# Kernel tuning notes

Measured on AMD Instinct MI355X. Metric: run time of the kernel, lower is better.

## Reference

```python
import jax, jax.numpy as jnp
import numpy as np

B, C, H, W = 1, 512, 64, 64
HEADS, DIM_HEAD = 8, 64
GROUPS = 32
EPS = 1e-5
SCALE = DIM_HEAD ** -0.5


def setup_inputs() -> dict:
    key = jax.random.key(0)
    ks = jax.random.split(key, 8)
    inner = HEADS * DIM_HEAD  # 512
    s = 0.02
    return {
        "hidden_states": jax.random.normal(ks[0], (B, C, H, W), jnp.float32),
        "gn_gamma": jnp.ones((C,), jnp.float32),
        "gn_beta": jnp.zeros((C,), jnp.float32),
        "wq": jax.random.normal(ks[1], (inner, C), jnp.float32) * s,
        "wk": jax.random.normal(ks[2], (inner, C), jnp.float32) * s,
        "wv": jax.random.normal(ks[3], (inner, C), jnp.float32) * s,
        "wo": jax.random.normal(ks[4], (C, inner), jnp.float32) * s,
        "bo": jnp.zeros((C,), jnp.float32),
    }


def _group_norm(x, gamma, beta):
    # x: [B, C, H, W]; normalize within channel groups over (C//G, H, W)
    b, c, h, w = x.shape
    xg = x.reshape(b, GROUPS, c // GROUPS, h, w)
    mean = xg.mean(axis=(2, 3, 4), keepdims=True)
    var = xg.var(axis=(2, 3, 4), keepdims=True)
    xg = (xg - mean) * jax.lax.rsqrt(var + EPS)
    x = xg.reshape(b, c, h, w)
    return x * gamma[None, :, None, None] + beta[None, :, None, None]


def reference(hidden_states, gn_gamma, gn_beta, wq, wk, wv, wo, bo):
    residual = hidden_states
    x = _group_norm(hidden_states, gn_gamma, gn_beta)
    b, c, h, w = x.shape
    n = h * w
    x = x.reshape(b, c, n).transpose(0, 2, 1)  # [B, N, C]

    # torch Linear: y = x @ W^T (bias=False for q/k/v)
    q = (x @ wq.T).reshape(b, n, HEADS, DIM_HEAD).transpose(0, 2, 1, 3)  # [B,H,N,D]
    k = (x @ wk.T).reshape(b, n, HEADS, DIM_HEAD).transpose(0, 2, 1, 3)
    v = (x @ wv.T).reshape(b, n, HEADS, DIM_HEAD).transpose(0, 2, 1, 3)

    scores = jnp.einsum("bhqd,bhkd->bhqk", q, k) * SCALE  # [B,H,N,N]
    probs = jax.nn.softmax(scores, axis=-1)
    out = jnp.einsum("bhqk,bhkd->bhqd", probs, v)  # [B,H,N,D]

    out = out.transpose(0, 2, 1, 3).reshape(b, n, HEADS * DIM_HEAD)  # [B,N,inner]
    out = out @ wo.T + bo  # [B,N,C]
    out = out.transpose(0, 2, 1).reshape(b, c, h, w)
    return out + residual
```

## Files before the change

### kernel.cpp

```cpp
#include <hip/hip_runtime.h>

#define N_TOK 4096
#define C_DIM 512
#define NH    8
#define EPS   1e-5f
#define NSPLIT 4
#define THR   11.0f

typedef __attribute__((ext_vector_type(8))) __bf16 bf16x8;
typedef __attribute__((ext_vector_type(4))) float  f32x4;
using u16 = unsigned short;
using u32 = unsigned int;

#define MFMA16 __builtin_amdgcn_mfma_f32_16x16x32_bf16

__device__ __forceinline__ u16 f2bf(float f){
  u32 x = __builtin_bit_cast(u32, f);
  x += 0x7fffu + ((x>>16)&1u);
  return (u16)(x>>16);
}
__device__ __forceinline__ float bf2f(u16 v){
  return __builtin_bit_cast(float, (u32)v<<16);
}
__device__ __forceinline__ float exp2a(float x){
  float r; asm("v_exp_f32 %0, %1" : "=v"(r) : "v"(x)); return r;
}
__device__ __forceinline__ u32 cvtpk(float lo, float hi){
  u32 r; asm("v_cvt_pk_bf16_f32 %0, %1, %2" : "=v"(r) : "v"(lo), "v"(hi)); return r;
}
__device__ __forceinline__ float max3a(float a, float b, float c){
  float r; asm("v_max3_f32 %0, %1, %2, %3" : "=v"(r) : "v"(a), "v"(b), "v"(c)); return r;
}
__device__ __forceinline__ void dma16(const void* src, void* lds){
  __builtin_amdgcn_global_load_lds(
      (const __attribute__((address_space(1))) u32*)src,
      (__attribute__((address_space(3))) u32*)lds, 16, 0, 0);
}

__global__ __launch_bounds__(256) void k_pre(const float* __restrict__ s0,
      const float* __restrict__ s1, const float* __restrict__ s2,
      const float* __restrict__ s3, u16* __restrict__ d0, u16* __restrict__ d1,
      u16* __restrict__ d2, u16* __restrict__ d3,
      const float* __restrict__ x, float* __restrict__ pstat,
      u16* __restrict__ xbf){
  __shared__ float rs[4], rss[4];
  int b = blockIdx.x;
  if (b < 1024){
    int m = b >> 8;
    int i = (b & 255)*256 + threadIdx.x;
    const float* s = m==0?s0 : m==1?s1 : m==2?s2 : s3;
    u16*         d = m==0?d0 : m==1?d1 : m==2?d2 : d3;
    float4 v = ((const float4*)s)[i];
    ushort4 o; o.x=f2bf(v.x); o.y=f2bf(v.y); o.z=f2bf(v.z); o.w=f2bf(v.w);
    ((ushort4*)d)[i] = o;
    return;
  }
  int gb = b - 1024;
  int g = gb>>3, p = gb&7, t = threadIdx.x;
  const float4* gx4 = (const float4*)(x + (size_t)g*16*N_TOK) + (size_t)p*2048;
  ushort4* xb4 = (ushort4*)xbf + (size_t)g*16384 + (size_t)p*2048;
  float s=0.f, ss=0.f;
  #pragma unroll
  for (int k=0;k<8;k++){
    float4 v = gx4[t + k*256];
    s  += v.x+v.y+v.z+v.w;
    ss += v.x*v.x+v.y*v.y+v.z*v.z+v.w*v.w;
    ushort4 o; o.x=f2bf(v.x); o.y=f2bf(v.y); o.z=f2bf(v.z); o.w=f2bf(v.w);
    xb4[t + k*256] = o;
  }
  for (int m=1;m<64;m<<=1){ s += __shfl_xor(s,m); ss += __shfl_xor(ss,m); }
  int w=t>>6, lane=t&63;
  if (lane==0){ rs[w]=s; rss[w]=ss; }
  __syncthreads();
  if (t==0){
    pstat[(g*8+p)*2  ] = rs[0]+rs[1]+rs[2]+rs[3];
    pstat[(g*8+p)*2+1] = rss[0]+rss[1]+rss[2]+rss[3];
  }
}

__global__ __launch_bounds__(256) void k_gn_apply(const u16* __restrict__ xbf,
      const float* __restrict__ pstat, const float* __restrict__ gamma,
      const float* __restrict__ beta, u16* __restrict__ X){
  int g = blockIdx.x, c0 = g*16;
  int n = blockIdx.y*256 + threadIdx.x;
  float S=0.f, SS=0.f;
  #pragma unroll
  for (int p=0;p<8;p++){ S += pstat[(g*8+p)*2]; SS += pstat[(g*8+p)*2+1]; }
  float mean = S*(1.f/65536.f);
  float rstd = rsqrtf(SS*(1.f/65536.f) - mean*mean + EPS);
  u16 ov[16];
  #pragma unroll
  for (int c=0;c<16;c++){
    float gm = gamma[c0+c]*rstd;
    float be = beta[c0+c] - mean*gm;
    float v  = bf2f(xbf[(size_t)(c0+c)*N_TOK + n])*gm + be;
    ov[c] = f2bf(v);
  }
  uint4* dst = (uint4*)&X[(size_t)n*C_DIM + c0];
  dst[0] = *(uint4*)&ov[0];
  dst[1] = *(uint4*)&ov[8];
}

__device__ __forceinline__ void gemm_core64(const u16* A, const u16* B,
      int m0, int n0, char* LDS, f32x4 (&acc)[4][2]){
  int t = threadIdx.x, w = t>>6, l = t&63, lr = l&15, li = l>>4;
  int wr = w>>1, wc = w&1;
  char* As = LDS;
  char* Bs = LDS + 32768;
  const char* Ac = (const char*)A + (size_t)m0*1024;
  const char* Bc = (const char*)B + (size_t)n0*1024;
  int rswz = (lr&7)<<4;

  int rowA[4], segA[4], rowB[2], segB[2];
  #pragma unroll
  for (int k=0;k<4;k++){ int s=t+k*256; rowA[k]=s>>3; segA[k]=s&7; }
  #pragma unroll
  for (int k=0;k<2;k++){ int s=t+k*256; rowB[k]=s>>3; segB[k]=s&7; }

  #define STAGE(it, bb) { int koff=(it)*128;                                   \
    _Pragma("unroll")                                                          \
    for (int k=0;k<4;k++){                                                     \
      int ys = (segA[k]*16) ^ ((rowA[k]&7)<<4);                                \
      dma16(Ac + (size_t)rowA[k]*1024 + koff + ys,                             \
            As + (bb)*16384 + w*1024 + k*4096);                                \
    }                                                                          \
    _Pragma("unroll")                                                          \
    for (int k=0;k<2;k++){                                                     \
      int ys = (segB[k]*16) ^ ((rowB[k]&7)<<4);                                \
      dma16(Bc + (size_t)rowB[k]*1024 + koff + ys,                             \
            Bs + (bb)*8192 + w*1024 + k*4096);                                 \
    } }

  STAGE(0, 0);
  __syncthreads();

  int buf = 0;
  for (int it=0; it<8; it++){
    if (it < 7){ STAGE(it+1, buf^1); }
    char* Ab = As + buf*16384;
    char* Bb = Bs + buf*8192;
    #pragma unroll
    for (int ks=0; ks<2; ks++){
      bf16x8 af[4], bfr[2];
      #pragma unroll
      for (int i=0;i<4;i++){
        int ra = wr*64 + i*16 + lr;
        af[i]  = *(const bf16x8*)(Ab + ra*128 + ((li*16 + ks*64) ^ rswz));
      }
      #pragma unroll
      for (int j=0;j<2;j++){
        int rb = wc*32 + j*16 + lr;
        bfr[j] = *(const bf16x8*)(Bb + rb*128 + ((li*16 + ks*64) ^ rswz));
      }
      __builtin_amdgcn_s_setprio(1);
      #pragma unroll
      for (int i=0;i<4;i++){
        #pragma unroll
        for (int j=0;j<2;j++){
          acc[i][j] = MFMA16(af[i], bfr[j], acc[i][j], 0,0,0);
        }
      }
      __builtin_amdgcn_s_setprio(0);
    }
    __syncthreads();
    buf ^= 1;
  }
  #undef STAGE
}

__global__ __launch_bounds__(256,3) void k_qkv2(const u16* __restrict__ X,
      const u16* __restrict__ wq, const u16* __restrict__ wk,
      const u16* __restrict__ wv, u16* __restrict__ Qo, u16* __restrict__ Ko,
      u16* __restrict__ Vto){
  __shared__ char LDS[49152];
  int b = blockIdx.x;
  const u16 *A, *B; u16* Cp; int ldc, m0, n0; float sc = 1.f; bool vperm = false;
  if (b < 256){        A=X;  B=wq; Cp=Qo;  ldc=512;  m0=(b>>3)*128; n0=(b&7)*64;
                       sc = 0.125f*1.44269504f; }
  else if (b < 512){ int r=b-256; A=X;  B=wk; Cp=Ko;  ldc=512;  m0=(r>>3)*128; n0=(r&7)*64; }
  else             { int r=b-512; A=wv; B=X;  Cp=Vto; ldc=4096; m0=(r>>6)*128; n0=(r&63)*64;
                     vperm = true; }

  f32x4 acc[4][2] = {};
  gemm_core64(A, B, m0, n0, LDS, acc);

  int t = threadIdx.x, w = t>>6, l = t&63, lr = l&15, li = l>>4;
  int wr = w>>1, wc = w&1;
  #pragma unroll
  for (int i=0;i<4;i++){
    #pragma unroll
    for (int rr=0;rr<4;rr++){
      int mm = m0 + wr*64 + i*16 + li*4 + rr;
      #pragma unroll
      for (int j=0;j<2;j++){
        int nn = n0 + wc*32 + j*16 + lr;
        if (vperm){
          int tl = nn & 63;
          int pos = (tl & 35) | ((tl & 12) << 1) | ((tl & 16) >> 2);
          nn = (nn & ~63) | pos;
        }
        Cp[(size_t)mm*ldc + nn] = f2bf(acc[i][j][rr]*sc);
      }
    }
  }
}

__global__ __launch_bounds__(256,3) void k_oproj2(const u16* __restrict__ Wo,
      const u16* __restrict__ Ob, const float* __restrict__ bo,
      const float* __restrict__ res, float* __restrict__ out){
  __shared__ char LDS[49152];
  int b = blockIdx.x;
  int m0 = (b>>6)*128, n0 = (b&63)*64;

  f32x4 acc[4][2] = {};
  gemm_core64(Wo, Ob, m0, n0, LDS, acc);

  int t = threadIdx.x, w = t>>6, l = t&63, lr = l&15, li = l>>4;
  int wr = w>>1, wc = w&1;
  #pragma unroll
  for (int i=0;i<4;i++){
    #pragma unroll
    for (int rr=0;rr<4;rr++){
      int cc = m0 + wr*64 + i*16 + li*4 + rr;
      float bias = bo[cc];
      #pragma unroll
      for (int j=0;j<2;j++){
        int nn = n0 + wc*32 + j*16 + lr;
        size_t off = (size_t)cc*4096 + nn;
        out[off] = acc[i][j][rr] + bias + res[off];
      }
    }
  }
}

__global__ __launch_bounds__(512,8) void k_attn8(const u16* __restrict__ Q,
      const u16* __restrict__ K, const u16* __restrict__ Vt,
      u16* __restrict__ Opart, float* __restrict__ ml){
  __shared__ char KV[2][16384];
  int b = blockIdx.x;
  int xcd  = b & 7;
  int slot = b >> 3;
  int pair = xcd*4 + (slot >> 5);
  int h  = pair & 7;
  int sp = pair >> 3;
  int q0 = (slot & 31) * 128;
  int t = threadIdx.x, w = t>>6, l = t&63, lr = l&15, li = l>>4;
  char* KVb = (char*)KV;
  int qbase = q0 + w*16;

  const u16* Qp = Q + (size_t)(qbase + lr)*512 + h*64 + li*8;
  bf16x8 qa0 = *(const bf16x8*)(Qp);
  bf16x8 qa1 = *(const bf16x8*)(Qp + 32);

  int row = t>>3, seg = t&7;
  int ys  = (seg*16) ^ ((row&7)<<4);
  const char* ksrc = (const char*)K  + (size_t)(sp*1024 + row)*1024 + h*128 + ys;
  const char* vsrc = (const char*)Vt + (size_t)(h*64 + row)*8192 + sp*2048 + ys;
  int ldso = w*1024;

  dma16(ksrc, KVb + ldso);
  dma16(vsrc, KVb + 8192 + ldso);
  __syncthreads();

  f32x4 acc[4] = {};
  float m0=-1e30f, l0=0.f;
  int buf = 0;

  for (int it=0; it<16; it++){
    if (it < 15){
      int nb = buf^1;
      dma16(ksrc + (size_t)(it+1)*65536, KVb + nb*16384 + ldso);
      dma16(vsrc + (it+1)*128,           KVb + nb*16384 + 8192 + ldso);
    }
    char* Klb = KVb + buf*16384;
    char* Vlb = Klb + 8192;

    f32x4 st[4] = {};
    __builtin_amdgcn_s_setprio(1);
    #pragma unroll
    for (int T=0;T<4;T++){
      int krow = T*16 + lr, swz = (krow&7)<<4;
      const char* rb = Klb + krow*128;
      bf16x8 k0 = *(const bf16x8*)(rb + ((li*16     ) ^ swz));
      bf16x8 k1 = *(const bf16x8*)(rb + ((li*16 + 64) ^ swz));
      st[T] = MFMA16(k0, qa0, st[T], 0,0,0);
      st[T] = MFMA16(k1, qa1, st[T], 0,0,0);
    }
    __builtin_amdgcn_s_setprio(0);

    u32 pk[8];
    {
      float a0 = max3a(st[0][0],st[0][1],st[0][2]);
      float a1 = max3a(st[1][0],st[1][1],st[1][2]);
      float a2 = max3a(st[2][0],st[2][1],st[2][2]);
      float a3 = max3a(st[3][0],st[3][1],st[3][2]);
      float b0 = max3a(st[0][3],st[1][3],st[2][3]);
      float pmax = fmaxf(max3a(a0,a1,a2), max3a(a3,b0,st[3][3]));
      pmax = fmaxf(pmax, __shfl_xor(pmax,16));
      pmax = fmaxf(pmax, __shfl_xor(pmax,32));
      if (!__all(pmax <= m0 + THR)){
        float mnew = fmaxf(m0, pmax);
        float fac = exp2a(m0 - mnew);
        m0 = mnew; l0 *= fac;
        float f0=__shfl(fac, li*20+0), f1=__shfl(fac, li*20+1);
        float f2=__shfl(fac, li*20+2), f3=__shfl(fac, li*20+3);
        #pragma unroll
        for (int T=0;T<4;T++){
          acc[T][0]*=f0; acc[T][1]*=f1; acc[T][2]*=f2; acc[T][3]*=f3;
        }
      }
      float lad = 0.f;
      #pragma unroll
      for (int T=0;T<4;T++){
        float p0=exp2a(st[T][0]-m0), p1=exp2a(st[T][1]-m0);
        float p2=exp2a(st[T][2]-m0), p3=exp2a(st[T][3]-m0);
        lad += (p0+p1)+(p2+p3);
        pk[T*2]   = cvtpk(p0,p1);
        pk[T*2+1] = cvtpk(p2,p3);
      }
      l0 += lad;
    }

    __builtin_amdgcn_s_setprio(1);
    #pragma unroll
    for (int c=0;c<2;c++){
      union { bf16x8 v; u32 u[4]; } A0;
      #pragma unroll
      for (int k=0;k<4;k++){ A0.u[k]=pk[c*4+k]; }
      #pragma unroll
      for (int T=0;T<4;T++){
        int vrow = T*16 + lr, vswz = (vrow&7)<<4;
        bf16x8 vb = *(const bf16x8*)(Vlb + vrow*128 + ((c*64 + li*16) ^ vswz));
        acc[T] = MFMA16(A0.v, vb, acc[T], 0,0,0);
      }
    }
    __builtin_amdgcn_s_setprio(0);

    __syncthreads();
    buf ^= 1;
  }

  l0 += __shfl_xor(l0,16); l0 += __shfl_xor(l0,32);
  u16* Op = Opart + (size_t)sp*N_TOK*C_DIM;
  #pragma unroll
  for (int T=0;T<4;T++){
    #pragma unroll
    for (int r=0;r<4;r++){
      Op[(size_t)(qbase + li*4 + r)*512 + h*64 + T*16 + lr] = f2bf(acc[T][r]);
    }
  }
  if (li==0){
    float* p0 = ml + (((size_t)sp*NH + h)*N_TOK + qbase + lr)*2;
    p0[0]=m0; p0[1]=l0;
  }
}

__global__ __launch_bounds__(256) void k_merge2(const u16* __restrict__ Opart,
      const float* __restrict__ ml, u16* __restrict__ Ob){
  int i  = blockIdx.x*256 + threadIdx.x;
  int q  = i >> 7;
  int c4 = i & 127;
  int h  = c4 >> 4;
  float m[NSPLIT], lv[NSPLIT];
  #pragma unroll
  for (int s=0;s<NSPLIT;s++){
    const float* p = ml + (((size_t)s*NH + h)*N_TOK + q)*2;
    m[s]=p[0]; lv[s]=p[1];
  }
  float M = fmaxf(max3a(m[0],m[1],m[2]), m[3]);
  float wgt[NSPLIT]; float L = 0.f;
  #pragma unroll
  for (int s=0;s<NSPLIT;s++){ wgt[s] = exp2a(m[s]-M); L += lv[s]*wgt[s]; }
  float inv = 1.f/L;
  float4 o = {0.f,0.f,0.f,0.f};
  #pragma unroll
  for (int s=0;s<NSPLIT;s++){
    ushort4 a = ((const ushort4*)(Opart + (size_t)s*N_TOK*C_DIM))[i];
    o.x += bf2f(a.x)*wgt[s]; o.y += bf2f(a.y)*wgt[s];
    o.z += bf2f(a.z)*wgt[s]; o.w += bf2f(a.w)*wgt[s];
  }
  ushort4 r;
  r.x=f2bf(o.x*inv); r.y=f2bf(o.y*inv); r.z=f2bf(o.z*inv); r.w=f2bf(o.w*inv);
  ((ushort4*)Ob)[i] = r;
}

extern "C" void kernel_launch(void* const* d_in, const int* in_sizes, int n_in,
                              void* d_out, int out_size, void* d_ws, size_t ws_size,
                              hipStream_t stream){
  (void)in_sizes; (void)n_in; (void)out_size; (void)ws_size;
  const float* hs    = (const float*)d_in[0];
  const float* gamma = (const float*)d_in[1];
  const float* beta  = (const float*)d_in[2];
  const float* wq    = (const float*)d_in[3];
  const float* wk    = (const float*)d_in[4];
  const float* wv    = (const float*)d_in[5];
  const float* wo    = (const float*)d_in[6];
  const float* bo    = (const float*)d_in[7];
  float* out = (float*)d_out;

  u16* X   = (u16*)d_ws;
  u16* Qb  = X   + (size_t)4096*512;
  u16* Kb  = Qb  + (size_t)4096*512;
  u16* Vtb = Kb  + (size_t)4096*512;
  u16* Ob  = Vtb + (size_t)4096*512;
  u16* xbf = Ob  + (size_t)4096*512;
  u16* wqb = xbf + (size_t)4096*512;
  u16* wkb = wqb + (size_t)512*512;
  u16* wvb = wkb + (size_t)512*512;
  u16* wob = wvb + (size_t)512*512;
  float* pstat = (float*)(wob + (size_t)512*512);
  u16* Opart   = (u16*)(pstat + 1024);
  float* mlbuf = (float*)(Opart + (size_t)NSPLIT*4096*512);

  k_pre<<<1280,256,0,stream>>>(wq, wk, wv, wo, wqb, wkb, wvb, wob, hs, pstat, xbf);
  dim3 ga(32, 16);
  k_gn_apply<<<ga,256,0,stream>>>(xbf, pstat, gamma, beta, X);
  k_qkv2<<<768,256,0,stream>>>(X, wqb, wkb, wvb, Qb, Kb, Vtb);
  k_attn8<<<1024,512,0,stream>>>(Qb, Kb, Vtb, Opart, mlbuf);
  k_merge2<<<2048,256,0,stream>>>(Opart, mlbuf, Ob);
  k_oproj2<<<256,256,0,stream>>>(wob, Ob, bo, hs, out);
}
```

Baseline: 90.92 us.

## Process four query sub-tiles per wave in attention to reuse K/V fragments

The attention kernel now gives each wave 64 query rows, held as four 16-row sub-tiles, instead of 16. Each block has 4 waves and 256 queries, and the grid shrinks from 1024 to 512 blocks. K and V fragments are loaded from LDS once per iteration into registers and reused across the four sub-tiles, cutting LDS read traffic per query. The costs are much higher register use (16 accumulator tiles plus 16 K/V fragments), lower occupancy, and fewer blocks to fill the GPU.

After: 88.24 us. 1.03x faster.

```diff
diff --git a/kernel.cpp b/kernel.cpp
--- a/kernel.cpp
+++ b/kernel.cpp
@@ -233,125 +233,158 @@
   }
 }
 
-__global__ __launch_bounds__(512,8) void k_attn8(const u16* __restrict__ Q,
+__global__ __launch_bounds__(256,2) void k_attn9(const u16* __restrict__ Q,
       const u16* __restrict__ K, const u16* __restrict__ Vt,
       u16* __restrict__ Opart, float* __restrict__ ml){
   __shared__ char KV[2][16384];
   int b = blockIdx.x;
   int xcd  = b & 7;
   int slot = b >> 3;
-  int pair = xcd*4 + (slot >> 5);
+  int pair = xcd*4 + (slot >> 4);
   int h  = pair & 7;
   int sp = pair >> 3;
-  int q0 = (slot & 31) * 128;
+  int q0 = (slot & 15) * 256;
   int t = threadIdx.x, w = t>>6, l = t&63, lr = l&15, li = l>>4;
   char* KVb = (char*)KV;
-  int qbase = q0 + w*16;
+  int qbase = q0 + w*64;
 
   const u16* Qp = Q + (size_t)(qbase + lr)*512 + h*64 + li*8;
-  bf16x8 qa0 = *(const bf16x8*)(Qp);
-  bf16x8 qa1 = *(const bf16x8*)(Qp + 32);
-
-  int row = t>>3, seg = t&7;
-  int ys  = (seg*16) ^ ((row&7)<<4);
-  const char* ksrc = (const char*)K  + (size_t)(sp*1024 + row)*1024 + h*128 + ys;
-  const char* vsrc = (const char*)Vt + (size_t)(h*64 + row)*8192 + sp*2048 + ys;
-  int ldso = w*1024;
-
-  dma16(ksrc, KVb + ldso);
-  dma16(vsrc, KVb + 8192 + ldso);
+  bf16x8 qa[4][2];
+  #pragma unroll
+  for (int s=0;s<4;s++){
+    qa[s][0] = *(const bf16x8*)(Qp + (size_t)s*16*512);
+    qa[s][1] = *(const bf16x8*)(Qp + (size_t)s*16*512 + 32);
+  }
+
+  int srow = l>>3, y0 = (l&7)*16;
+  const char* Kc = (const char*)K;
+  const char* Vc = (const char*)Vt;
+  const char* ksrc[2]; const char* vsrc[2]; int ldso[2];
+  #pragma unroll
+  for (int j=0;j<2;j++){
+    int row = w*16 + j*8 + srow;
+    int ys  = y0 ^ ((row&7)<<4);
+    ksrc[j] = Kc + (size_t)(sp*1024 + row)*1024 + h*128 + ys;
+    vsrc[j] = Vc + (size_t)(h*64 + row)*8192 + sp*2048 + ys;
+    ldso[j] = w*2048 + j*1024;
+  }
+
+  #pragma unroll
+  for (int j=0;j<2;j++){
+    dma16(ksrc[j], KVb + ldso[j]);
+    dma16(vsrc[j], KVb + 8192 + ldso[j]);
+  }
   __syncthreads();
 
-  f32x4 acc[4] = {};
-  float m0=-1e30f, l0=0.f;
+  f32x4 acc[4][4] = {};
+  float m[4] = {-1e30f,-1e30f,-1e30f,-1e30f};
+  float lsum[4] = {0.f,0.f,0.f,0.f};
   int buf = 0;
 
   for (int it=0; it<16; it++){
     if (it < 15){
       int nb = buf^1;
-      dma16(ksrc + (size_t)(it+1)*65536, KVb + nb*16384 + ldso);
-      dma16(vsrc + (it+1)*128,           KVb + nb*16384 + 8192 + ldso);
+      #pragma unroll
+      for (int j=0;j<2;j++){
+        dma16(ksrc[j] + (size_t)(it+1)*65536, KVb + nb*16384 + ldso[j]);
+        dma16(vsrc[j] + (it+1)*128,           KVb + nb*16384 + 8192 + ldso[j]);
+      }
     }
     char* Klb = KVb + buf*16384;
     char* Vlb = Klb + 8192;
 
-    f32x4 st[4] = {};
-    __builtin_amdgcn_s_setprio(1);
+    bf16x8 k0[4], k1[4], vf[2][4];
     #pragma unroll
     for (int T=0;T<4;T++){
-      int krow = T*16 + lr, swz = (krow&7)<<4;
-      const char* rb = Klb + krow*128;
-      bf16x8 k0 = *(const bf16x8*)(rb + ((li*16     ) ^ swz));
-      bf16x8 k1 = *(const bf16x8*)(rb + ((li*16 + 64) ^ swz));
-      st[T] = MFMA16(k0, qa0, st[T], 0,0,0);
-      st[T] = MFMA16(k1, qa1, st[T], 0,0,0);
-    }
-    __builtin_amdgcn_s_setprio(0);
-
-    u32 pk[8];
-    {
-      float a0 = max3a(st[0][0],st[0][1],st[0][2]);
-      float a1 = max3a(st[1][0],st[1][1],st[1][2]);
-      float a2 = max3a(st[2][0],st[2][1],st[2][2]);
-      float a3 = max3a(st[3][0],st[3][1],st[3][2]);
-      float b0 = max3a(st[0][3],st[1][3],st[2][3]);
-      float pmax = fmaxf(max3a(a0,a1,a2), max3a(a3,b0,st[3][3]));
-      pmax = fmaxf(pmax, __shfl_xor(pmax,16));
-      pmax = fmaxf(pmax, __shfl_xor(pmax,32));
-      if (!__all(pmax <= m0 + THR)){
-        float mnew = fmaxf(m0, pmax);
-        float fac = exp2a(m0 - mnew);
-        m0 = mnew; l0 *= fac;
-        float f0=__shfl(fac, li*20+0), f1=__shfl(fac, li*20+1);
-        float f2=__shfl(fac, li*20+2), f3=__shfl(fac, li*20+3);
+      int row = T*16 + lr, swz = (row&7)<<4;
+      const char* rb = Klb + row*128;
+      k0[T] = *(const bf16x8*)(rb + ((li*16     ) ^ swz));
+      k1[T] = *(const bf16x8*)(rb + ((li*16 + 64) ^ swz));
+      const char* vb = Vlb + row*128;
+      vf[0][T] = *(const bf16x8*)(vb + ((     li*16) ^ swz));
+      vf[1][T] = *(const bf16x8*)(vb + ((64 + li*16) ^ swz));
+    }
+
+    #pragma unroll
+    for (int s=0;s<4;s++){
+      f32x4 st[4] = {};
+      __builtin_amdgcn_s_setprio(1);
+      #pragma unroll
+      for (int T=0;T<4;T++){
+        st[T] = MFMA16(k0[T], qa[s][0], st[T], 0,0,0);
+        st[T] = MFMA16(k1[T], qa[s][1], st[T], 0,0,0);
+      }
+      __builtin_amdgcn_s_setprio(0);
+
+      u32 pk[8];
+      {
+        float a0 = max3a(st[0][0],st[0][1],st[0][2]);
+        float a1 = max3a(st[1][0],st[1][1],st[1][2]);
+        float a2 = max3a(st[2][0],st[2][1],st[2][2]);
+        float a3 = max3a(st[3][0],st[3][1],st[3][2]);
+        float b0 = max3a(st[0][3],st[1][3],st[2][3]);
+        float pmax = fmaxf(max3a(a0,a1,a2), max3a(a3,b0,st[3][3]));
+        pmax = fmaxf(pmax, __shfl_xor(pmax,16));
+        pmax = fmaxf(pmax, __shfl_xor(pmax,32));
+        if (!__all(pmax <= m[s] + THR)){
+          float mnew = fmaxf(m[s], pmax);
+          float fac = exp2a(m[s] - mnew);
+          m[s] = mnew; lsum[s] *= fac;
+          float f0=__shfl(fac, li*20+0), f1=__shfl(fac, li*20+1);
+          float f2=__shfl(fac, li*20+2), f3=__shfl(fac, li*20+3);
+          #pragma unroll
+          for (int T=0;T<4;T++){
+            acc[s][T][0]*=f0; acc[s][T][1]*=f1;
+            acc[s][T][2]*=f2; acc[s][T][3]*=f3;
+          }
+        }
+        float lad = 0.f;
         #pragma unroll
         for (int T=0;T<4;T++){
-          acc[T][0]*=f0; acc[T][1]*=f1; acc[T][2]*=f2; acc[T][3]*=f3;
+          float p0=exp2a(st[T][0]-m[s]), p1=exp2a(st[T][1]-m[s]);
+          float p2=exp2a(st[T][2]-m[s]), p3=exp2a(st[T][3]-m[s]);
+          lad += (p0+p1)+(p2+p3);
+          pk[T*2]   = cvtpk(p0,p1);
+          pk[T*2+1] = cvtpk(p2,p3);
         }
-      }
-      float lad = 0.f;
-      #pragma unroll
-      for (int T=0;T<4;T++){
-        float p0=exp2a(st[T][0]-m0), p1=exp2a(st[T][1]-m0);
-        float p2=exp2a(st[T][2]-m0), p3=exp2a(st[T][3]-m0);
-        lad += (p0+p1)+(p2+p3);
-        pk[T*2]   = cvtpk(p0,p1);
-        pk[T*2+1] = cvtpk(p2,p3);
-      }
-      l0 += lad;
-    }
-
-    __builtin_amdgcn_s_setprio(1);
-    #pragma unroll
-    for (int c=0;c<2;c++){
-      union { bf16x8 v; u32 u[4]; } A0;
-      #pragma unroll
-      for (int k=0;k<4;k++){ A0.u[k]=pk[c*4+k]; }
-      #pragma unroll
-      for (int T=0;T<4;T++){
-        int vrow = T*16 + lr, vswz = (vrow&7)<<4;
-        bf16x8 vb = *(const bf16x8*)(Vlb + vrow*128 + ((c*64 + li*16) ^ vswz));
-        acc[T] = MFMA16(A0.v, vb, acc[T], 0,0,0);
-      }
-    }
-    __builtin_amdgcn_s_setprio(0);
+        lsum[s] += lad;
+      }
+
+      __builtin_amdgcn_s_setprio(1);
+      #pragma unroll
+      for (int c=0;c<2;c++){
+        union { bf16x8 v; u32 u[4]; } A0;
+        #pragma unroll
+        for (int k=0;k<4;k++){ A0.u[k]=pk[c*4+k]; }
+        #pragma unroll
+        for (int T=0;T<4;T++){
+          acc[s][T] = MFMA16(A0.v, vf[c][T], acc[s][T], 0,0,0);
+        }
+      }
+      __builtin_amdgcn_s_setprio(0);
+    }
 
     __syncthreads();
     buf ^= 1;
   }
 
-  l0 += __shfl_xor(l0,16); l0 += __shfl_xor(l0,32);
   u16* Op = Opart + (size_t)sp*N_TOK*C_DIM;
   #pragma unroll
-  for (int T=0;T<4;T++){
-    #pragma unroll
-    for (int r=0;r<4;r++){
-      Op[(size_t)(qbase + li*4 + r)*512 + h*64 + T*16 + lr] = f2bf(acc[T][r]);
-    }
-  }
-  if (li==0){
-    float* p0 = ml + (((size_t)sp*NH + h)*N_TOK + qbase + lr)*2;
-    p0[0]=m0; p0[1]=l0;
+  for (int s=0;s<4;s++){
+    lsum[s] += __shfl_xor(lsum[s],16);
+    lsum[s] += __shfl_xor(lsum[s],32);
+    #pragma unroll
+    for (int T=0;T<4;T++){
+      #pragma unroll
+      for (int r=0;r<4;r++){
+        Op[(size_t)(qbase + s*16 + li*4 + r)*512 + h*64 + T*16 + lr]
+            = f2bf(acc[s][T][r]);
+      }
+    }
+    if (li==0){
+      float* p0 = ml + (((size_t)sp*NH + h)*N_TOK + qbase + s*16 + lr)*2;
+      p0[0]=m[s]; p0[1]=lsum[s];
+    }
   }
 }
 
@@ -416,7 +449,7 @@
   dim3 ga(32, 16);
   k_gn_apply<<<ga,256,0,stream>>>(xbf, pstat, gamma, beta, X);
   k_qkv2<<<768,256,0,stream>>>(X, wqb, wkb, wvb, Qb, Kb, Vtb);
-  k_attn8<<<1024,512,0,stream>>>(Qb, Kb, Vtb, Opart, mlbuf);
+  k_attn9<<<512,256,0,stream>>>(Qb, Kb, Vtb, Opart, mlbuf);
   k_merge2<<<2048,256,0,stream>>>(Opart, mlbuf, Ob);
   k_oproj2<<<256,256,0,stream>>>(wob, Ob, bo, hs, out);
 }
```
